# Kernel optimization log

Measured on AMD Instinct MI355X. Metric: run time of the kernel, lower is better.

## Reference

```python
import jax, jax.numpy as jnp
import numpy as np

B, S, D = 4, 2048, 2048


def setup_inputs() -> dict:
    key = jax.random.key(0)
    ks = jax.random.split(key, 24)
    sc = 1.0 / np.sqrt(D)
    def lin(ki, kb):
        W = jax.random.normal(ks[ki], (D, D), dtype=jnp.float32) * sc
        b = jax.random.normal(ks[kb], (D,), dtype=jnp.float32) * 0.01
        return W, b
    Wi, bWi = lin(0, 1); Ui, bUi = lin(2, 3)
    Wf, bWf = lin(4, 5); Uf, bUf = lin(6, 7)
    Wc, bWc = lin(8, 9); Uc, bUc = lin(10, 11)
    Wo, bWo = lin(12, 13); Uo, bUo = lin(14, 15)
    Wp, bp = lin(16, 17)
    x = jax.random.normal(ks[18], (B, S, D), dtype=jnp.float32)
    h = jax.random.normal(ks[19], (B, S, D), dtype=jnp.float32)
    return dict(x=x, h=h, Wi=Wi, bWi=bWi, Ui=Ui, bUi=bUi,
                Wf=Wf, bWf=bWf, Uf=Uf, bUf=bUf,
                Wc=Wc, bWc=bWc, Uc=Uc, bUc=bUc,
                Wo=Wo, bWo=bWo, Uo=Uo, bUo=bUo,
                Wp=Wp, bp=bp)


def reference(x, h, Wi, bWi, Ui, bUi, Wf, bWf, Uf, bUf,
              Wc, bWc, Uc, bUc, Wo, bWo, Uo, bUo, Wp, bp):
    # In the torch source, h[:, t, :] is read BEFORE being overwritten at step t,
    # and c is zero-initialized with each slot written once (so f * c_prev == 0).
    # Hence the computation is exactly parallel over the time axis.
    Zi = jnp.einsum('bsd,ed->bse', x, Wi) + bWi + jnp.einsum('bsd,ed->bse', h, Ui) + bUi
    Zf = jnp.einsum('bsd,ed->bse', x, Wf) + bWf + jnp.einsum('bsd,ed->bse', h, Uf) + bUf
    Zc = jnp.einsum('bsd,ed->bse', x, Wc) + bWc + jnp.einsum('bsd,ed->bse', h, Uc) + bUc
    Zo = jnp.einsum('bsd,ed->bse', x, Wo) + bWo + jnp.einsum('bsd,ed->bse', h, Uo) + bUo
    i = jnp.exp(Zi)
    f = jnp.exp(Zf)  # multiplies a zero cell state in the source; kept for fidelity
    c = f * jnp.zeros_like(f) + i * jnp.tanh(Zc)
    h_out = jax.nn.sigmoid(Zo) * jnp.tanh(c)
    hidden_state = h_out[:, -1, :] @ Wp.T + bp
    return (hidden_state, c)
```

## Files before the change

kernel.cpp:

```cpp
#include <hip/hip_runtime.h>
#include <hip/hip_bf16.h>

typedef short short8 __attribute__((ext_vector_type(8)));
typedef unsigned short ushort8v __attribute__((ext_vector_type(8)));
typedef float f32x4 __attribute__((ext_vector_type(4)));

#define D_DIM 2048
#define KTOT 4096
#define M_TOT 8192
#define NPACK 4096


__device__ __forceinline__ unsigned short f2bf(float f) {
    union { float f; unsigned u; } c; c.f = f;
    unsigned u = c.u;
    u += 0x7fffu + ((u >> 16) & 1u);
    return (unsigned short)(u >> 16);
}

__device__ __forceinline__ float fast_tanh(float x) {
    float ax = fabsf(x);
    float ez = __expf(2.0f * fminf(ax, 15.0f));
    float t = (ez - 1.0f) / (ez + 1.0f);
    return copysignf(t, x);
}

#define GLOAD_LDS16(g, l)                                                     \
    __builtin_amdgcn_global_load_lds(                                         \
        (const __attribute__((address_space(1))) void*)(g),                   \
        (__attribute__((address_space(3))) void*)(l), 16, 0, 0)


__global__ __launch_bounds__(256)
void pack2(const float* __restrict__ X, const float* __restrict__ H,
           __hip_bfloat16* __restrict__ dst, int total8) {
    int t = blockIdx.x * 256 + threadIdx.x;
    if (t >= total8) return;
    long e0 = (long)t * 8;
    long r  = e0 >> 12;
    int  k  = (int)(e0 & 4095);
    const float* src = (k < D_DIM) ? (X + r * D_DIM + k)
                                   : (H + r * D_DIM + (k - D_DIM));
    float4 v0 = *(const float4*)(src);
    float4 v1 = *(const float4*)(src + 4);
    ushort8v o;
    o[0] = f2bf(v0.x); o[1] = f2bf(v0.y); o[2] = f2bf(v0.z); o[3] = f2bf(v0.w);
    o[4] = f2bf(v1.x); o[5] = f2bf(v1.y); o[6] = f2bf(v1.z); o[7] = f2bf(v1.w);
    *(ushort8v*)(dst + e0) = o;
}


__global__ __launch_bounds__(256)
void pack_gates(const float* __restrict__ Wi, const float* __restrict__ Ui,
                const float* __restrict__ Wc, const float* __restrict__ Uc,
                __hip_bfloat16* __restrict__ dst) {
    int t = blockIdx.x * 256 + threadIdx.x;
    const int g = t >> 9;
    const int k = (t & 511) * 8;
    const int w = g & 31;
    const int n = ((g >> 5) << 4) | (w & 15);
    const float* Wm = (w & 16) ? Wc : Wi;
    const float* Um = (w & 16) ? Uc : Ui;
    const float* src = (k < D_DIM) ? (Wm + (size_t)n * D_DIM + k)
                                   : (Um + (size_t)n * D_DIM + (k - D_DIM));
    float4 v0 = *(const float4*)(src);
    float4 v1 = *(const float4*)(src + 4);
    ushort8v o;
    o[0] = f2bf(v0.x); o[1] = f2bf(v0.y); o[2] = f2bf(v0.z); o[3] = f2bf(v0.w);
    o[4] = f2bf(v1.x); o[5] = f2bf(v1.y); o[6] = f2bf(v1.z); o[7] = f2bf(v1.w);
    *(ushort8v*)(dst + (size_t)g * KTOT + k) = o;
}


#define BK 64
#define NT (KTOT / BK)

__device__ __forceinline__ void mfma16(f32x4 (&acc)[8][4], int mb,
                                       const short8 (&a)[4], const short8 (&b)[4]) {
    #pragma unroll
    for (int m = 0; m < 4; ++m)
        #pragma unroll
        for (int n = 0; n < 4; ++n)
            acc[mb + m][n] = __builtin_amdgcn_mfma_f32_16x16x32_bf16(
                a[m], b[n], acc[mb + m][n], 0, 0, 0);
}

#define READ4(dst, base, IMM)                                                 \
    { _Pragma("unroll")                                                       \
      for (int m_ = 0; m_ < 4; ++m_)                                          \
          dst[m_] = *(const short8*)((base) + (IMM) + m_ * 1024); }

#define STAGE2(g0, g1, ldsbase, DIMM, KB)                                     \
    { GLOAD_LDS16((g0) + (KB), (ldsbase) + (DIMM) + dOff);                    \
      GLOAD_LDS16((g1) + (KB), (ldsbase) + (DIMM) + dOff + 1024); }

#define TILE(CUROFF, NXTOFF, PF)                                              \
  {                                                                           \
       \
    READ4(aQ, rdA, (CUROFF) + 4096);                                          \
    if (PF) { STAGE2(gA0, gA1, ldsA, (NXTOFF), kb);                           \
              asm volatile("s_waitcnt vmcnt(2)" ::: "memory"); }              \
    else    { asm volatile("s_waitcnt vmcnt(0)" ::: "memory"); }              \
    __builtin_amdgcn_s_barrier();                                             \
    asm volatile("s_waitcnt lgkmcnt(4)" ::: "memory");                        \
    __builtin_amdgcn_sched_barrier(0);                                        \
    __builtin_amdgcn_s_setprio(1); mfma16(acc, 0, aP, bP);                    \
    __builtin_amdgcn_s_setprio(0);                                            \
         \
    READ4(aP, rdA, (CUROFF) + 16384);                                         \
    READ4(bQ, rdB, (CUROFF) + 16384);                                         \
    if (PF) STAGE2(gB0, gB1, ldsB, (NXTOFF), kb);                             \
    __builtin_amdgcn_s_barrier();                                             \
    asm volatile("s_waitcnt lgkmcnt(8)" ::: "memory");                        \
    __builtin_amdgcn_sched_barrier(0);                                        \
    __builtin_amdgcn_s_setprio(1); mfma16(acc, 4, aQ, bP);                    \
    __builtin_amdgcn_s_setprio(0);                                            \
       \
    READ4(aQ, rdA, (CUROFF) + 16384 + 4096);                                  \
    if (PF) { STAGE2(gA0, gA1, ldsA, (NXTOFF) + 16384, kb + 64);              \
              asm volatile("s_waitcnt vmcnt(2)" ::: "memory"); }              \
    else    { asm volatile("s_waitcnt vmcnt(0)" ::: "memory"); }              \
    __builtin_amdgcn_s_barrier();                                             \
    asm volatile("s_waitcnt lgkmcnt(4)" ::: "memory");                        \
    __builtin_amdgcn_sched_barrier(0);                                        \
    __builtin_amdgcn_s_setprio(1); mfma16(acc, 0, aP, bQ);                    \
    __builtin_amdgcn_s_setprio(0);                                            \
         \
    if (PF) { READ4(aP, rdA, (NXTOFF));                                       \
              READ4(bP, rdB, (NXTOFF));                                       \
              STAGE2(gB0, gB1, ldsB, (NXTOFF) + 16384, kb + 64); }            \
    __builtin_amdgcn_s_barrier();                                             \
    if (PF) asm volatile("s_waitcnt lgkmcnt(8)" ::: "memory");                \
    else    asm volatile("s_waitcnt lgkmcnt(0)" ::: "memory");                \
    __builtin_amdgcn_sched_barrier(0);                                        \
    __builtin_amdgcn_s_setprio(1); mfma16(acc, 4, aQ, bQ);                    \
    __builtin_amdgcn_s_setprio(0);                                            \
  }

__global__ __launch_bounds__(512, 2)
void gemm8(const __hip_bfloat16* __restrict__ A,
           const __hip_bfloat16* __restrict__ Bp,
           const float* __restrict__ bWi, const float* __restrict__ bUi,
           const float* __restrict__ bWc, const float* __restrict__ bUc,
           float* __restrict__ Cout) {
    __shared__ __hip_bfloat16 sA[2][2][256][32];
    __shared__ __hip_bfloat16 sB[2][2][256][32];

    const int tid  = threadIdx.x;
    const int wid  = tid >> 6;
    const int lane = tid & 63;

    int bid = blockIdx.x;
    bid = (bid & 7) * 64 + (bid >> 3);
    const int tn = (bid & 15) * 256;
    const int tm = (bid >> 4) * 256;

    const int wr  = (wid >> 2) * 128;
    const int wc  = (wid & 3) * 64;
    const int r15 = lane & 15;
    const int uswz16 = (((lane >> 4) ^ ((r15 >> 1) & 3)) * 16);

    const int Lb0  = wid * 128 + lane;
    const int row0 = Lb0 >> 2;
    const int u0   = (Lb0 & 3) ^ ((Lb0 >> 3) & 3);
    const char* gA0 = (const char*)(A  + (size_t)(tm + row0) * KTOT) + u0 * 16;
    const char* gA1 = gA0 + (size_t)16 * KTOT * 2;
    const char* gB0 = (const char*)(Bp + (size_t)(tn + row0) * KTOT) + u0 * 16;
    const char* gB1 = gB0 + (size_t)16 * KTOT * 2;
    char* ldsA = (char*)sA;
    char* ldsB = (char*)sB;
    const int dOff = Lb0 * 16;

    const char* rdA = (const char*)sA + (wr + r15) * 64 + uswz16;
    const char* rdB = (const char*)sB + (wc + r15) * 64 + uswz16;

    f32x4 acc[8][4] = {};
    short8 aP[4], aQ[4], bP[4], bQ[4];

    STAGE2(gA0, gA1, ldsA, 0, 0);
    STAGE2(gB0, gB1, ldsB, 0, 0);
    STAGE2(gA0, gA1, ldsA, 16384, 64);
    STAGE2(gB0, gB1, ldsB, 16384, 64);
    asm volatile("s_waitcnt vmcnt(4)" ::: "memory");
    __builtin_amdgcn_s_barrier();
    READ4(aP, rdA, 0);
    READ4(bP, rdB, 0);

    int kb = 128;
    #pragma unroll 1
    for (int it = 0; it < 31; ++it) {
        TILE(0, 32768, 1); kb += 128;
        TILE(32768, 0, 1); kb += 128;
    }
    TILE(0, 32768, 1); kb += 128;
    TILE(32768, 0, 0);

    const int rg4 = (lane >> 4) * 4;
    #pragma unroll
    for (int q = 0; q < 2; ++q) {
        const int gn = (tn >> 1) + (wc >> 1) + q * 16 + r15;
        const float bi_ = bWi[gn] + bUi[gn];
        const float bc_ = bWc[gn] + bUc[gn];
        #pragma unroll
        for (int m = 0; m < 8; ++m) {
            const int gm = tm + wr + m * 16 + rg4;
            #pragma unroll
            for (int r = 0; r < 4; ++r) {
                const float zi = acc[m][2 * q][r]     + bi_;
                const float zc = acc[m][2 * q + 1][r] + bc_;
                Cout[(size_t)(gm + r) * D_DIM + gn] = __expf(zi) * fast_tanh(zc);
            }
        }
    }
}


__global__ __launch_bounds__(256)
void last_gate(const float* __restrict__ x, const float* __restrict__ h,
               const float* __restrict__ Wo, const float* __restrict__ bWo,
               const float* __restrict__ Uo, const float* __restrict__ bUo,
               const float* __restrict__ cfull, float* __restrict__ hbuf) {
    const int o    = blockIdx.x * 4 + (threadIdx.x >> 6);
    const int lane = threadIdx.x & 63;
    const int b = o >> 11, e = o & 2047;
    const float* xr = x  + ((size_t)b * D_DIM + (D_DIM - 1)) * D_DIM;
    const float* hr = h  + ((size_t)b * D_DIM + (D_DIM - 1)) * D_DIM;
    const float* wo = Wo + (size_t)e * D_DIM;
    const float* uo = Uo + (size_t)e * D_DIM;
    float s = 0.0f;
    for (int d = lane; d < D_DIM; d += 64)
        s += xr[d] * wo[d] + hr[d] * uo[d];
    #pragma unroll
    for (int off = 32; off; off >>= 1) s += __shfl_down(s, off);
    if (lane == 0) {
        const float zo  = s + bWo[e] + bUo[e];
        const float sig = 1.0f / (1.0f + __expf(-zo));
        const float cv  = cfull[((size_t)b * D_DIM + (D_DIM - 1)) * D_DIM + e];
        hbuf[o] = sig * fast_tanh(cv);
    }
}


__global__ __launch_bounds__(256)
void proj(const float* __restrict__ hbuf, const float* __restrict__ Wp,
          const float* __restrict__ bp, float* __restrict__ out) {
    const int o    = blockIdx.x * 4 + (threadIdx.x >> 6);
    const int lane = threadIdx.x & 63;
    const int b = o >> 11, p = o & 2047;
    const float* hv = hbuf + (size_t)b * D_DIM;
    const float* wp = Wp   + (size_t)p * D_DIM;
    float s = 0.0f;
    for (int e = lane; e < D_DIM; e += 64)
        s += hv[e] * wp[e];
    #pragma unroll
    for (int off = 32; off; off >>= 1) s += __shfl_down(s, off);
    if (lane == 0) out[o] = s + bp[p];
}


extern "C" void kernel_launch(void* const* d_in, const int* in_sizes, int n_in,
                              void* d_out, int out_size, void* d_ws, size_t ws_size,
                              hipStream_t stream) {
    const float* x   = (const float*)d_in[0];
    const float* h   = (const float*)d_in[1];
    const float* Wi  = (const float*)d_in[2];  const float* bWi = (const float*)d_in[3];
    const float* Ui  = (const float*)d_in[4];  const float* bUi = (const float*)d_in[5];
    const float* Wc  = (const float*)d_in[10]; const float* bWc = (const float*)d_in[11];
    const float* Uc  = (const float*)d_in[12]; const float* bUc = (const float*)d_in[13];
    const float* Wo  = (const float*)d_in[14]; const float* bWo = (const float*)d_in[15];
    const float* Uo  = (const float*)d_in[16]; const float* bUo = (const float*)d_in[17];
    const float* Wp  = (const float*)d_in[18]; const float* bp  = (const float*)d_in[19];

    float* out = (float*)d_out;
    char*  ws  = (char*)d_ws;

    __hip_bfloat16* Abf  = (__hip_bfloat16*)ws;
    __hip_bfloat16* Bpk  = (__hip_bfloat16*)(ws + ((size_t)64 << 20));
    float*          hbuf = (float*)(ws + ((size_t)96 << 20));

    pack2<<<16384, 256, 0, stream>>>(x, h, Abf, M_TOT * KTOT / 8);
    pack_gates<<<8192, 256, 0, stream>>>(Wi, Ui, Wc, Uc, Bpk);

    gemm8<<<(M_TOT / 256) * (NPACK / 256), 512, 0, stream>>>(
        Abf, Bpk, bWi, bUi, bWc, bUc, out + 8192);

    last_gate<<<2048, 256, 0, stream>>>(x, h, Wo, bWo, Uo, bUo, out + 8192,
                                        (float*)hbuf);
    proj<<<2048, 256, 0, stream>>>(hbuf, Wp, bp, out);
}
```

Measured before the change: 356.1 us.

## Deepen global-to-LDS prefetch to three half-tiles in flight

Restructures the GEMM main loop so global-to-LDS loads run one more 64-wide K slice ahead. The prologue stages three slices instead of two, and each tile refills the buffer region just consumed. The vmcnt waits are relaxed to 6 so more loads stay outstanding and global latency is hidden better. The risk is a WAR hazard on the LDS region being refilled, which relies on barrier placement, plus subtle correctness in the tail tiles.

After: 333.2 us. 6.4% less time.

```diff
diff --git a/kernel.cpp b/kernel.cpp
--- a/kernel.cpp
+++ b/kernel.cpp
@@ -29,6 +29,11 @@
     __builtin_amdgcn_global_load_lds(                                         \
         (const __attribute__((address_space(1))) void*)(g),                   \
         (__attribute__((address_space(3))) void*)(l), 16, 0, 0)
+
+#define WAITVM_(N) asm volatile("s_waitcnt vmcnt(" #N ")" ::: "memory")
+#define WAITVM(N)  WAITVM_(N)
+#define WAITLG_(N) asm volatile("s_waitcnt lgkmcnt(" #N ")" ::: "memory")
+#define WAITLG(N)  WAITLG_(N)
 
 
 __global__ __launch_bounds__(256)
@@ -90,48 +95,47 @@
       for (int m_ = 0; m_ < 4; ++m_)                                          \
           dst[m_] = *(const short8*)((base) + (IMM) + m_ * 1024); }
 
-#define STAGE2(g0, g1, ldsbase, DIMM, KB)                                     \
-    { GLOAD_LDS16((g0) + (KB), (ldsbase) + (DIMM) + dOff);                    \
-      GLOAD_LDS16((g1) + (KB), (ldsbase) + (DIMM) + dOff + 1024); }
-
-#define TILE(CUROFF, NXTOFF, PF)                                              \
+#define STAGE_A(DIMM, KB)                                                     \
+    { GLOAD_LDS16(gA0 + (KB), ldsA + (DIMM) + dOff);                          \
+      GLOAD_LDS16(gA1 + (KB), ldsA + (DIMM) + dOff + 1024); }
+#define STAGE_B(DIMM, KB)                                                     \
+    { GLOAD_LDS16(gB0 + (KB), ldsB + (DIMM) + dOff);                          \
+      GLOAD_LDS16(gB1 + (KB), ldsB + (DIMM) + dOff + 1024); }
+
+#define TILE(CUR, NXT, V1, V3, ST12, ST34, PF4)                               \
   {                                                                           \
-       \
-    READ4(aQ, rdA, (CUROFF) + 4096);                                          \
-    if (PF) { STAGE2(gA0, gA1, ldsA, (NXTOFF), kb);                           \
-              asm volatile("s_waitcnt vmcnt(2)" ::: "memory"); }              \
-    else    { asm volatile("s_waitcnt vmcnt(0)" ::: "memory"); }              \
-    __builtin_amdgcn_s_barrier();                                             \
-    asm volatile("s_waitcnt lgkmcnt(4)" ::: "memory");                        \
+                    \
+    READ4(aQ, rdA, (CUR) + 4096);                                             \
+    if (ST12) STAGE_A((NXT) + 16384, kb + 64);                                \
+    WAITVM(V1);                                                               \
+    __builtin_amdgcn_s_barrier();                                             \
+    WAITLG(4);                                                                \
     __builtin_amdgcn_sched_barrier(0);                                        \
     __builtin_amdgcn_s_setprio(1); mfma16(acc, 0, aP, bP);                    \
     __builtin_amdgcn_s_setprio(0);                                            \
-         \
-    READ4(aP, rdA, (CUROFF) + 16384);                                         \
-    READ4(bQ, rdB, (CUROFF) + 16384);                                         \
-    if (PF) STAGE2(gB0, gB1, ldsB, (NXTOFF), kb);                             \
-    __builtin_amdgcn_s_barrier();                                             \
-    asm volatile("s_waitcnt lgkmcnt(8)" ::: "memory");                        \
+           \
+    READ4(aP, rdA, (CUR) + 16384);                                            \
+    READ4(bQ, rdB, (CUR) + 16384);                                            \
+    if (ST12) STAGE_B((NXT) + 16384, kb + 64);                                \
+    __builtin_amdgcn_s_barrier();                                             \
+    WAITLG(8);                                                                \
     __builtin_amdgcn_sched_barrier(0);                                        \
     __builtin_amdgcn_s_setprio(1); mfma16(acc, 4, aQ, bP);                    \
     __builtin_amdgcn_s_setprio(0);                                            \
-       \
-    READ4(aQ, rdA, (CUROFF) + 16384 + 4096);                                  \
-    if (PF) { STAGE2(gA0, gA1, ldsA, (NXTOFF) + 16384, kb + 64);              \
-              asm volatile("s_waitcnt vmcnt(2)" ::: "memory"); }              \
-    else    { asm volatile("s_waitcnt vmcnt(0)" ::: "memory"); }              \
-    __builtin_amdgcn_s_barrier();                                             \
-    asm volatile("s_waitcnt lgkmcnt(4)" ::: "memory");                        \
+                    \
+    READ4(aQ, rdA, (CUR) + 16384 + 4096);                                     \
+    if (ST34) STAGE_A((CUR), kb + 128);                                       \
+    WAITVM(V3);                                                               \
+    __builtin_amdgcn_s_barrier();                                             \
+    WAITLG(4);                                                                \
     __builtin_amdgcn_sched_barrier(0);                                        \
     __builtin_amdgcn_s_setprio(1); mfma16(acc, 0, aP, bQ);                    \
     __builtin_amdgcn_s_setprio(0);                                            \
-         \
-    if (PF) { READ4(aP, rdA, (NXTOFF));                                       \
-              READ4(bP, rdB, (NXTOFF));                                       \
-              STAGE2(gB0, gB1, ldsB, (NXTOFF) + 16384, kb + 64); }            \
-    __builtin_amdgcn_s_barrier();                                             \
-    if (PF) asm volatile("s_waitcnt lgkmcnt(8)" ::: "memory");                \
-    else    asm volatile("s_waitcnt lgkmcnt(0)" ::: "memory");                \
+      \
+    if (PF4) { READ4(aP, rdA, (NXT)); READ4(bP, rdB, (NXT)); }                \
+    if (ST34) STAGE_B((CUR), kb + 128);                                       \
+    __builtin_amdgcn_s_barrier();                                             \
+    if (PF4) { WAITLG(8); } else { WAITLG(0); }                               \
     __builtin_amdgcn_sched_barrier(0);                                        \
     __builtin_amdgcn_s_setprio(1); mfma16(acc, 4, aQ, bQ);                    \
     __builtin_amdgcn_s_setprio(0);                                            \
@@ -177,11 +181,10 @@
     f32x4 acc[8][4] = {};
     short8 aP[4], aQ[4], bP[4], bQ[4];
 
-    STAGE2(gA0, gA1, ldsA, 0, 0);
-    STAGE2(gB0, gB1, ldsB, 0, 0);
-    STAGE2(gA0, gA1, ldsA, 16384, 64);
-    STAGE2(gB0, gB1, ldsB, 16384, 64);
-    asm volatile("s_waitcnt vmcnt(4)" ::: "memory");
+    STAGE_A(0, 0);        STAGE_B(0, 0);
+    STAGE_A(16384, 64);   STAGE_B(16384, 64);
+    STAGE_A(32768, 128);  STAGE_B(32768, 128);
+    WAITVM(8);
     __builtin_amdgcn_s_barrier();
     READ4(aP, rdA, 0);
     READ4(bP, rdB, 0);
@@ -189,11 +192,11 @@
     int kb = 128;
     #pragma unroll 1
     for (int it = 0; it < 31; ++it) {
-        TILE(0, 32768, 1); kb += 128;
-        TILE(32768, 0, 1); kb += 128;
+        TILE(0, 32768, 6, 6, 1, 1, 1); kb += 128;
+        TILE(32768, 0, 6, 6, 1, 1, 1); kb += 128;
     }
-    TILE(0, 32768, 1); kb += 128;
-    TILE(32768, 0, 0);
+    TILE(0, 32768, 6, 4, 1, 0, 1); kb += 128;
+    TILE(32768, 0, 0, 0, 0, 0, 0);
 
     const int rg4 = (lane >> 4) * 4;
     #pragma unroll
```
